# Performance work log

Hardware: AMD Instinct MI355X
Metric: run time of the kernel (lower is better)

The kernel has to match this reference:

```python
import jax, jax.numpy as jnp
import numpy as np

EPS_MSG = 1e-7   # GENConv message eps
EPS_LN = 1e-5    # LayerNorm eps

N, F_IN, D, D_OUT = 32768, 64, 512, 128


def setup_inputs() -> dict:
    key = jax.random.key(0)
    ks = jax.random.split(key, 20)
    s = 0.02
    inp = {
        "batch": jax.random.normal(ks[0], (1, N, F_IN), jnp.float32),
        "W_enc": jax.random.normal(ks[1], (F_IN, D), jnp.float32) * s,
        "b_enc": jnp.zeros((D,), jnp.float32),
        "Wf": jax.random.normal(ks[2], (D, D_OUT), jnp.float32) * s,
        "bf": jnp.zeros((D_OUT,), jnp.float32),
    }
    for l in range(2):
        inp[f"t{l}"] = jnp.array(1.0, jnp.float32)           # learnable softmax temperature
        inp[f"W1_{l}"] = jax.random.normal(ks[3 + 6 * l], (D, 2 * D), jnp.float32) * s
        inp[f"b1_{l}"] = jnp.zeros((2 * D,), jnp.float32)
        inp[f"g_{l}"] = jnp.ones((2 * D,), jnp.float32)      # LN gamma
        inp[f"be_{l}"] = jnp.zeros((2 * D,), jnp.float32)    # LN beta
        inp[f"W2_{l}"] = jax.random.normal(ks[4 + 6 * l], (2 * D, D), jnp.float32) * s
        inp[f"b2_{l}"] = jnp.zeros((D,), jnp.float32)
    return inp


def _layer_norm(z, g, b):
    mu = jnp.mean(z, axis=-1, keepdims=True)
    var = jnp.var(z, axis=-1, keepdims=True)
    return (z - mu) * jax.lax.rsqrt(var + EPS_LN) * g + b


def _deepgcn_layer(x, t, W1, b1, g, be, W2, b2):
    # res+ block: h = conv(act(norm(x))); return x + h   (norm is Identity here)
    h = jax.nn.relu(x)                       # [n, d]
    # GENConv with complete graph: msg_j = relu(h_j) + eps (independent of target i)
    m = jax.nn.relu(h) + EPS_MSG             # [n, d]
    alpha = jax.nn.softmax(t * m, axis=0)    # per-channel softmax over all source nodes
    agg = jnp.sum(alpha * m, axis=0)         # [d]  -- identical for every target node
    out = h + agg[None, :]                   # + x_dst residual inside GENConv
    # GENConv MLP: Linear(d,2d) -> LayerNorm -> ReLU -> Linear(2d,d)
    z = jax.nn.relu(_layer_norm(out @ W1 + b1, g, be))
    out = z @ W2 + b2
    return x + out


def reference(batch, W_enc, b_enc, Wf, bf,
              t0, W1_0, b1_0, g_0, be_0, W2_0, b2_0,
              t1, W1_1, b1_1, g_1, be_1, W2_1, b2_1):
    bsz, n, _ = batch.shape
    x = batch.reshape(bsz * n, -1) @ W_enc + b_enc   # node encoder
    x = _deepgcn_layer(x, t0, W1_0, b1_0, g_0, be_0, W2_0, b2_0)
    x = _deepgcn_layer(x, t1, W1_1, b1_1, g_1, be_1, W2_1, b2_1)
    x = jax.nn.relu(x)                               # layers[0].act(layers[0].norm(x)), norm=Identity
    out = x @ Wf + bf
    return out.reshape(bsz, n, -1)
```

## Files before the change

### kernel.cpp

```cpp
#include <hip/hip_runtime.h>

#define DEV __device__ __forceinline__

typedef __attribute__((ext_vector_type(8))) short s8v;
typedef __attribute__((ext_vector_type(4))) float f4v;

DEV short f2bf(float f) {
  unsigned u = __builtin_bit_cast(unsigned, f);
  u += 0x7fffu + ((u >> 16) & 1u);
  return (short)(u >> 16);
}
DEV float bf2f(short s) {
  unsigned u = ((unsigned)(unsigned short)s) << 16;
  return __builtin_bit_cast(float, u);
}

DEV f4v mfma_16x16x32_bf16(s8v a, s8v b, f4v c) {
  asm("v_mfma_f32_16x16x32_bf16 %0, %1, %2, %0" : "+v"(c) : "v"(a), "v"(b));
  return c;
}

DEV s8v relu8(s8v a) {
#pragma unroll
  for (int i = 0; i < 8; ++i) a[i] = a[i] > (short)0 ? a[i] : (short)0;
  return a;
}

__global__ __launch_bounds__(256) void tconv_k(const float* __restrict__ in,
                                               short* __restrict__ out,
                                               int K, int N) {
  __shared__ float t[64][65];
  const int nb = blockIdx.x * 64, kb = blockIdx.y * 64;
  const int c = threadIdx.x & 63, r0 = threadIdx.x >> 6;
#pragma unroll
  for (int rr = 0; rr < 64; rr += 4)
    t[rr + r0][c] = in[(size_t)(kb + rr + r0) * N + nb + c];
  __syncthreads();
#pragma unroll
  for (int rr = 0; rr < 64; rr += 4)
    out[(size_t)(nb + rr + r0) * K + kb + c] = f2bf(t[c][rr + r0]);
}

__global__ __launch_bounds__(256) void conv_k(const float* __restrict__ in,
                                              short* __restrict__ out, int n4) {
  int i = blockIdx.x * 256 + threadIdx.x;
  if (i >= n4) return;
  float4 v = ((const float4*)in)[i];
  short4 o;
  o.x = f2bf(v.x);
  o.y = f2bf(v.y);
  o.z = f2bf(v.z);
  o.w = f2bf(v.w);
  ((short4*)out)[i] = o;
}

__global__ __launch_bounds__(256) void zero_k(float* p, int n) {
  int i = blockIdx.x * 256 + threadIdx.x;
  if (i < n) p[i] = 0.f;
}

__global__ __launch_bounds__(256) void finalize_k(const float* __restrict__ sums,
                                                  const float* __restrict__ W1,
                                                  const float* __restrict__ b1,
                                                  float* __restrict__ biasEff) {
  __shared__ float agg[512];
  const int tid = threadIdx.x;
  for (int d = tid; d < 512; d += 256) agg[d] = sums[512 + d] / sums[d];
  __syncthreads();
  const int j = blockIdx.x * 256 + tid;
  float a = b1[j];
  for (int d = 0; d < 512; ++d) a += agg[d] * W1[(size_t)d * 1024 + j];
  biasEff[j] = a;
}

__global__ __launch_bounds__(256) void ln_relu_k(short* __restrict__ z,
                                                 const float* __restrict__ g,
                                                 const float* __restrict__ be) {
  const int row = blockIdx.x * 4 + (threadIdx.x >> 6);
  const int lane = threadIdx.x & 63;
  short* zr = z + (size_t)row * 1024;
  s8v c0 = *(const s8v*)&zr[lane * 8];
  s8v c1 = *(const s8v*)&zr[512 + lane * 8];
  float v[16];
  float s = 0.f, q = 0.f;
#pragma unroll
  for (int i = 0; i < 8; ++i) { v[i] = bf2f(c0[i]); v[8 + i] = bf2f(c1[i]); }
#pragma unroll
  for (int i = 0; i < 16; ++i) { s += v[i]; q += v[i] * v[i]; }
#pragma unroll
  for (int o = 32; o > 0; o >>= 1) { s += __shfl_xor(s, o); q += __shfl_xor(q, o); }
  float mu = s * (1.f / 1024.f);
  float var = q * (1.f / 1024.f) - mu * mu;
  float rs = rsqrtf(var + 1e-5f);
  float gv[16], bv[16];
#pragma unroll
  for (int i = 0; i < 8; ++i) {
    gv[i] = g[lane * 8 + i];      gv[8 + i] = g[512 + lane * 8 + i];
    bv[i] = be[lane * 8 + i];     bv[8 + i] = be[512 + lane * 8 + i];
  }
  s8v o0, o1;
#pragma unroll
  for (int i = 0; i < 8; ++i) {
    o0[i] = f2bf(fmaxf((v[i] - mu) * rs * gv[i] + bv[i], 0.f));
    o1[i] = f2bf(fmaxf((v[8 + i] - mu) * rs * gv[8 + i] + bv[8 + i], 0.f));
  }
  *(s8v*)&zr[lane * 8] = o0;
  *(s8v*)&zr[512 + lane * 8] = o1;
}

#define F_ADD   1
#define F_WF32  2
#define F_WBF   4
#define F_SM    8
#define F_RELUA 16

template <int FLAGS>
__global__ __launch_bounds__(256) void gemm_k(const short* __restrict__ A,
                                              const short* __restrict__ Bt,
                                              const float* __restrict__ bias,
                                              const short* __restrict__ Xin,
                                              short* __restrict__ Cb,
                                              float* __restrict__ Cf,
                                              const float* __restrict__ tptr,
                                              float* __restrict__ sums,
                                              int M, int N, int K) {
  __shared__ short lA[128 * 32];
  __shared__ short lB[128 * 32];
  const int tid = threadIdx.x;
  const int lane = tid & 63, wid = tid >> 6;
  const int wr = wid >> 1, wc = wid & 1;
  const int nwg = gridDim.x * gridDim.y;
  const int wg = blockIdx.y * gridDim.x + blockIdx.x;
  const int swz = (wg & 7) * (nwg >> 3) + (wg >> 3);
  const int bx = swz % gridDim.x, by = swz / gridDim.x;
  const int brow = by * 128, bcol = bx * 128;
  const int l15 = lane & 15, lhi = lane >> 4;
  f4v acc[4][4] = {};

  for (int k0 = 0; k0 < K; k0 += 32) {
#pragma unroll
    for (int r = 0; r < 2; ++r) {
      int chunk = r * 256 + wid * 64 + lane;
      int row = chunk >> 2;
      int sw = (row & 3) ^ ((row >> 2) & 3);
      int kc = ((chunk & 3) ^ sw) << 3;
      const short* ga = A + (size_t)(brow + row) * K + (k0 + kc);
      const short* gb = Bt + (size_t)(bcol + row) * K + (k0 + kc);
      __builtin_amdgcn_global_load_lds(
          (const __attribute__((address_space(1))) void*)ga,
          (__attribute__((address_space(3))) void*)&lA[(r * 256 + wid * 64) * 8],
          16, 0, 0);
      __builtin_amdgcn_global_load_lds(
          (const __attribute__((address_space(1))) void*)gb,
          (__attribute__((address_space(3))) void*)&lB[(r * 256 + wid * 64) * 8],
          16, 0, 0);
    }
    __syncthreads();
    s8v af[4], bfr[4];
#pragma unroll
    for (int i = 0; i < 4; ++i) {
      const int rowA = wr * 64 + i * 16 + l15;
      const int sw = (rowA & 3) ^ ((rowA >> 2) & 3);
      const int co = (lhi ^ sw) << 3;
      af[i]  = *(const s8v*)&lA[rowA * 32 + co];
      bfr[i] = *(const s8v*)&lB[(wc * 64 + i * 16 + l15) * 32 + co];
      if (FLAGS & F_RELUA) af[i] = relu8(af[i]);
    }
#pragma unroll
    for (int mi = 0; mi < 4; ++mi)
#pragma unroll
      for (int ni = 0; ni < 4; ++ni)
        acc[mi][ni] = mfma_16x16x32_bf16(af[mi], bfr[ni], acc[mi][ni]);
    __syncthreads();
  }

  const float tv = (FLAGS & F_SM) ? tptr[0] : 0.f;
  float* sred = (float*)lA;
  if (FLAGS & F_SM) {
    sred[tid] = 0.f;
    __syncthreads();
  }
#pragma unroll
  for (int ni = 0; ni < 4; ++ni) {
    int col = bcol + wc * 64 + ni * 16 + l15;
    float bv = bias[col];
    float se = 0.f, sem = 0.f;
#pragma unroll
    for (int mi = 0; mi < 4; ++mi) {
#pragma unroll
      for (int r = 0; r < 4; ++r) {
        int row = brow + wr * 64 + mi * 16 + lhi * 4 + r;
        size_t idx = (size_t)row * N + col;
        float v = acc[mi][ni][r] + bv;
        if (FLAGS & F_ADD) v += bf2f(Xin[idx]);
        if (FLAGS & F_WF32) Cf[idx] = v;
        if (FLAGS & F_WBF) Cb[idx] = f2bf(v);
        if (FLAGS & F_SM) {
          float m = fmaxf(v, 0.f) + 1e-7f;
          float e = __expf(tv * m);
          se += e;
          sem += e * m;
        }
      }
    }
    if (FLAGS & F_SM) {
      se += __shfl_xor(se, 16);   se += __shfl_xor(se, 32);
      sem += __shfl_xor(sem, 16); sem += __shfl_xor(sem, 32);
      if (lhi == 0) {
        atomicAdd(&sred[wc * 64 + ni * 16 + l15], se);
        atomicAdd(&sred[128 + wc * 64 + ni * 16 + l15], sem);
      }
    }
  }
  if (FLAGS & F_SM) {
    __syncthreads();
    int v = tid >> 7, c = tid & 127;
    atomicAdd(&sums[v * 512 + bcol + c], sred[v * 128 + c]);
  }
}

extern "C" void kernel_launch(void* const* d_in, const int* in_sizes, int n_in,
                              void* d_out, int out_size, void* d_ws,
                              size_t ws_size, hipStream_t stream) {
  (void)in_sizes; (void)n_in; (void)out_size; (void)ws_size;
  const float* batch = (const float*)d_in[0];
  const float* W_enc = (const float*)d_in[1];
  const float* b_enc = (const float*)d_in[2];
  const float* Wf    = (const float*)d_in[3];
  const float* bfv   = (const float*)d_in[4];
  const float* tptr[2] = {(const float*)d_in[5],  (const float*)d_in[12]};
  const float* W1[2]   = {(const float*)d_in[6],  (const float*)d_in[13]};
  const float* b1[2]   = {(const float*)d_in[7],  (const float*)d_in[14]};
  const float* g[2]    = {(const float*)d_in[8],  (const float*)d_in[15]};
  const float* be[2]   = {(const float*)d_in[9],  (const float*)d_in[16]};
  const float* W2[2]   = {(const float*)d_in[10], (const float*)d_in[17]};
  const float* b2[2]   = {(const float*)d_in[11], (const float*)d_in[18]};
  float* out = (float*)d_out;

  const int M = 32768;
  char* ws = (char*)d_ws;
  size_t off = 0;
  auto alloc = [&](size_t bytes) -> char* {
    char* p = ws + off;
    off += (bytes + 255) & ~(size_t)255;
    return p;
  };
  short* xbf    = (short*)alloc((size_t)M * 512 * 2);
  short* zbuf   = (short*)alloc((size_t)M * 1024 * 2);
  short* bbuf   = (short*)alloc((size_t)M * 64 * 2);
  short* wencT  = (short*)alloc(512 * 64 * 2);
  short* w1T0   = (short*)alloc(1024 * 512 * 2);
  short* w2T0   = (short*)alloc(512 * 1024 * 2);
  short* w1T1   = (short*)alloc(1024 * 512 * 2);
  short* w2T1   = (short*)alloc(512 * 1024 * 2);
  short* wfT    = (short*)alloc(128 * 512 * 2);
  float* sums   = (float*)alloc(2 * 1024 * 4);
  float* biasEff= (float*)alloc(1024 * 4);
  short* w1T[2] = {w1T0, w1T1};
  short* w2T[2] = {w2T0, w2T1};

  tconv_k<<<dim3(512 / 64, 64 / 64), 256, 0, stream>>>(W_enc, wencT, 64, 512);
  tconv_k<<<dim3(1024 / 64, 512 / 64), 256, 0, stream>>>(W1[0], w1T[0], 512, 1024);
  tconv_k<<<dim3(512 / 64, 1024 / 64), 256, 0, stream>>>(W2[0], w2T[0], 1024, 512);
  tconv_k<<<dim3(1024 / 64, 512 / 64), 256, 0, stream>>>(W1[1], w1T[1], 512, 1024);
  tconv_k<<<dim3(512 / 64, 1024 / 64), 256, 0, stream>>>(W2[1], w2T[1], 1024, 512);
  tconv_k<<<dim3(128 / 64, 512 / 64), 256, 0, stream>>>(Wf, wfT, 512, 128);

  conv_k<<<(M * 64 / 4 + 255) / 256, 256, 0, stream>>>(batch, bbuf, M * 64 / 4);
  zero_k<<<(2048 + 255) / 256, 256, 0, stream>>>(sums, 2048);

  gemm_k<F_WBF | F_SM><<<dim3(512 / 128, M / 128), 256, 0, stream>>>(
      bbuf, wencT, b_enc, nullptr, xbf, nullptr, tptr[0], sums, M, 512, 64);

  for (int l = 0; l < 2; ++l) {
    finalize_k<<<4, 256, 0, stream>>>(sums + l * 1024, W1[l], b1[l], biasEff);
    gemm_k<F_WBF | F_RELUA><<<dim3(1024 / 128, M / 128), 256, 0, stream>>>(
        xbf, w1T[l], biasEff, nullptr, zbuf, nullptr, nullptr, nullptr,
        M, 1024, 512);
    ln_relu_k<<<M / 4, 256, 0, stream>>>(zbuf, g[l], be[l]);
    if (l == 0) {
      gemm_k<F_ADD | F_WBF | F_SM><<<dim3(512 / 128, M / 128), 256, 0, stream>>>(
          zbuf, w2T[l], b2[l], xbf, xbf, nullptr, tptr[1], sums + 1024,
          M, 512, 1024);
    } else {
      gemm_k<F_ADD | F_WBF><<<dim3(512 / 128, M / 128), 256, 0, stream>>>(
          zbuf, w2T[l], b2[l], xbf, xbf, nullptr, nullptr, nullptr,
          M, 512, 1024);
    }
  }

  gemm_k<F_WF32 | F_RELUA><<<dim3(128 / 128, M / 128), 256, 0, stream>>>(
      xbf, wfT, bfv, nullptr, nullptr, out, nullptr, nullptr, M, 128, 512);
}
```

Before: 431.7 us.

## Shrink GEMM tile to 64x128 and parallelize finalize bias reduction

The GEMM block tile drops from 128x128 to 64x128, with each of the four waves computing a 64x32 sub-tile instead of 64x64, which doubles the number of workgroups. This targets low occupancy and wave-quantization on the small-N GEMMs, such as the final 128-column projection that previously had only 256 blocks. The cost is lower arithmetic intensity per block: B tiles are reloaded twice as often per row. The finalize kernel also moves from 4 blocks with serial 512-long dot products to 64 blocks that split the K dimension across thread groups and reduce partials in shared memory.

After: 432.0 us. No clear change (+0.1%).

```diff
diff --git a/kernel.cpp b/kernel.cpp
--- a/kernel.cpp
+++ b/kernel.cpp
@@ -64,13 +64,26 @@
                                                   const float* __restrict__ b1,
                                                   float* __restrict__ biasEff) {
   __shared__ float agg[512];
+  __shared__ float part[16][16];
   const int tid = threadIdx.x;
   for (int d = tid; d < 512; d += 256) agg[d] = sums[512 + d] / sums[d];
   __syncthreads();
-  const int j = blockIdx.x * 256 + tid;
-  float a = b1[j];
-  for (int d = 0; d < 512; ++d) a += agg[d] * W1[(size_t)d * 1024 + j];
-  biasEff[j] = a;
+  const int j = blockIdx.x * 16 + (tid & 15);
+  const int grp = tid >> 4;
+  float p = 0.f;
+#pragma unroll 4
+  for (int dd = 0; dd < 32; ++dd) {
+    int d = grp * 32 + dd;
+    p += agg[d] * W1[(size_t)d * 1024 + j];
+  }
+  part[grp][tid & 15] = p;
+  __syncthreads();
+  if (tid < 16) {
+    float a = b1[blockIdx.x * 16 + tid];
+#pragma unroll
+    for (int g = 0; g < 16; ++g) a += part[g][tid];
+    biasEff[blockIdx.x * 16 + tid] = a;
+  }
 }
 
 __global__ __launch_bounds__(256) void ln_relu_k(short* __restrict__ z,
@@ -124,52 +137,59 @@
                                               const float* __restrict__ tptr,
                                               float* __restrict__ sums,
                                               int M, int N, int K) {
-  __shared__ short lA[128 * 32];
+  __shared__ short lA[64 * 32];
   __shared__ short lB[128 * 32];
   const int tid = threadIdx.x;
   const int lane = tid & 63, wid = tid >> 6;
-  const int wr = wid >> 1, wc = wid & 1;
   const int nwg = gridDim.x * gridDim.y;
   const int wg = blockIdx.y * gridDim.x + blockIdx.x;
   const int swz = (wg & 7) * (nwg >> 3) + (wg >> 3);
   const int bx = swz % gridDim.x, by = swz / gridDim.x;
-  const int brow = by * 128, bcol = bx * 128;
+  const int brow = by * 64, bcol = bx * 128;
   const int l15 = lane & 15, lhi = lane >> 4;
-  f4v acc[4][4] = {};
+  f4v acc[4][2] = {};
 
   for (int k0 = 0; k0 < K; k0 += 32) {
+    {
+      int chunk = wid * 64 + lane;
+      int row = chunk >> 2;
+      int sw = (row & 3) ^ ((row >> 2) & 3);
+      int kc = ((chunk & 3) ^ sw) << 3;
+      __builtin_amdgcn_global_load_lds(
+          (const __attribute__((address_space(1))) void*)(A + (size_t)(brow + row) * K + k0 + kc),
+          (__attribute__((address_space(3))) void*)&lA[(wid * 64) * 8],
+          16, 0, 0);
+    }
 #pragma unroll
     for (int r = 0; r < 2; ++r) {
       int chunk = r * 256 + wid * 64 + lane;
       int row = chunk >> 2;
       int sw = (row & 3) ^ ((row >> 2) & 3);
       int kc = ((chunk & 3) ^ sw) << 3;
-      const short* ga = A + (size_t)(brow + row) * K + (k0 + kc);
-      const short* gb = Bt + (size_t)(bcol + row) * K + (k0 + kc);
       __builtin_amdgcn_global_load_lds(
-          (const __attribute__((address_space(1))) void*)ga,
-          (__attribute__((address_space(3))) void*)&lA[(r * 256 + wid * 64) * 8],
-          16, 0, 0);
-      __builtin_amdgcn_global_load_lds(
-          (const __attribute__((address_space(1))) void*)gb,
+          (const __attribute__((address_space(1))) void*)(Bt + (size_t)(bcol + row) * K + k0 + kc),
           (__attribute__((address_space(3))) void*)&lB[(r * 256 + wid * 64) * 8],
           16, 0, 0);
     }
     __syncthreads();
-    s8v af[4], bfr[4];
+    s8v af[4], bfr[2];
 #pragma unroll
     for (int i = 0; i < 4; ++i) {
-      const int rowA = wr * 64 + i * 16 + l15;
+      const int rowA = i * 16 + l15;
       const int sw = (rowA & 3) ^ ((rowA >> 2) & 3);
-      const int co = (lhi ^ sw) << 3;
-      af[i]  = *(const s8v*)&lA[rowA * 32 + co];
-      bfr[i] = *(const s8v*)&lB[(wc * 64 + i * 16 + l15) * 32 + co];
+      af[i] = *(const s8v*)&lA[rowA * 32 + ((lhi ^ sw) << 3)];
       if (FLAGS & F_RELUA) af[i] = relu8(af[i]);
     }
 #pragma unroll
+    for (int j = 0; j < 2; ++j) {
+      const int rowB = wid * 32 + j * 16 + l15;
+      const int sw = (rowB & 3) ^ ((rowB >> 2) & 3);
+      bfr[j] = *(const s8v*)&lB[rowB * 32 + ((lhi ^ sw) << 3)];
+    }
+#pragma unroll
     for (int mi = 0; mi < 4; ++mi)
 #pragma unroll
-      for (int ni = 0; ni < 4; ++ni)
+      for (int ni = 0; ni < 2; ++ni)
         acc[mi][ni] = mfma_16x16x32_bf16(af[mi], bfr[ni], acc[mi][ni]);
     __syncthreads();
   }
@@ -181,15 +201,15 @@
     __syncthreads();
   }
 #pragma unroll
-  for (int ni = 0; ni < 4; ++ni) {
-    int col = bcol + wc * 64 + ni * 16 + l15;
+  for (int ni = 0; ni < 2; ++ni) {
+    int col = bcol + wid * 32 + ni * 16 + l15;
     float bv = bias[col];
     float se = 0.f, sem = 0.f;
 #pragma unroll
     for (int mi = 0; mi < 4; ++mi) {
 #pragma unroll
       for (int r = 0; r < 4; ++r) {
-        int row = brow + wr * 64 + mi * 16 + lhi * 4 + r;
+        int row = brow + mi * 16 + lhi * 4 + r;
         size_t idx = (size_t)row * N + col;
         float v = acc[mi][ni][r] + bv;
         if (FLAGS & F_ADD) v += bf2f(Xin[idx]);
@@ -207,8 +227,8 @@
       se += __shfl_xor(se, 16);   se += __shfl_xor(se, 32);
       sem += __shfl_xor(sem, 16); sem += __shfl_xor(sem, 32);
       if (lhi == 0) {
-        atomicAdd(&sred[wc * 64 + ni * 16 + l15], se);
-        atomicAdd(&sred[128 + wc * 64 + ni * 16 + l15], sem);
+        atomicAdd(&sred[wid * 32 + ni * 16 + l15], se);
+        atomicAdd(&sred[128 + wid * 32 + ni * 16 + l15], sem);
       }
     }
   }
@@ -269,26 +289,26 @@
   conv_k<<<(M * 64 / 4 + 255) / 256, 256, 0, stream>>>(batch, bbuf, M * 64 / 4);
   zero_k<<<(2048 + 255) / 256, 256, 0, stream>>>(sums, 2048);
 
-  gemm_k<F_WBF | F_SM><<<dim3(512 / 128, M / 128), 256, 0, stream>>>(
+  gemm_k<F_WBF | F_SM><<<dim3(512 / 128, M / 64), 256, 0, stream>>>(
       bbuf, wencT, b_enc, nullptr, xbf, nullptr, tptr[0], sums, M, 512, 64);
 
   for (int l = 0; l < 2; ++l) {
-    finalize_k<<<4, 256, 0, stream>>>(sums + l * 1024, W1[l], b1[l], biasEff);
-    gemm_k<F_WBF | F_RELUA><<<dim3(1024 / 128, M / 128), 256, 0, stream>>>(
+    finalize_k<<<64, 256, 0, stream>>>(sums + l * 1024, W1[l], b1[l], biasEff);
+    gemm_k<F_WBF | F_RELUA><<<dim3(1024 / 128, M / 64), 256, 0, stream>>>(
         xbf, w1T[l], biasEff, nullptr, zbuf, nullptr, nullptr, nullptr,
         M, 1024, 512);
     ln_relu_k<<<M / 4, 256, 0, stream>>>(zbuf, g[l], be[l]);
     if (l == 0) {
-      gemm_k<F_ADD | F_WBF | F_SM><<<dim3(512 / 128, M / 128), 256, 0, stream>>>(
+      gemm_k<F_ADD | F_WBF | F_SM><<<dim3(512 / 128, M / 64), 256, 0, stream>>>(
           zbuf, w2T[l], b2[l], xbf, xbf, nullptr, tptr[1], sums + 1024,
           M, 512, 1024);
     } else {
-      gemm_k<F_ADD | F_WBF><<<dim3(512 / 128, M / 128), 256, 0, stream>>>(
+      gemm_k<F_ADD | F_WBF><<<dim3(512 / 128, M / 64), 256, 0, stream>>>(
           zbuf, w2T[l], b2[l], xbf, xbf, nullptr, nullptr, nullptr,
           M, 512, 1024);
     }
   }
 
-  gemm_k<F_WF32 | F_RELUA><<<dim3(128 / 128, M / 128), 256, 0, stream>>>(
+  gemm_k<F_WF32 | F_RELUA><<<dim3(128 / 128, M / 64), 256, 0, stream>>>(
       xbf, wfT, bfv, nullptr, nullptr, out, nullptr, nullptr, M, 128, 512);
 }
```
